# Performance work log

Measured on AMD Instinct MI355X. Metric: run time of the kernel, lower is better.

Reference implementation:

```python
import jax, jax.numpy as jnp
import numpy as np

N_NODES = 100000
N_EDGES = 1600000
IN_DIM = 128
HID = 64
NUM_GRAPHS = 2048
NUM_CLASSES = 1


def setup_inputs() -> dict:
    key = jax.random.key(0)
    ks = jax.random.split(key, 16)
    x = jax.random.normal(ks[0], (N_NODES, IN_DIM), dtype=jnp.float32)
    edge_index = jax.random.randint(ks[1], (2, N_EDGES), 0, N_NODES, dtype=jnp.int64)
    batch_index = jnp.sort(jax.random.randint(ks[2], (N_NODES,), 0, NUM_GRAPHS, dtype=jnp.int64))
    # GCNConv weights (glorot-ish scale)
    def lin(k, fi, fo):
        return jax.random.normal(k, (fi, fo), dtype=jnp.float32) / np.sqrt(fi)
    W1 = lin(ks[3], IN_DIM, HID); b1 = jnp.zeros((HID,), jnp.float32)
    W2 = lin(ks[4], HID, HID);    b2 = jnp.zeros((HID,), jnp.float32)
    W3 = lin(ks[5], HID, HID);    b3 = jnp.zeros((HID,), jnp.float32)
    W4 = lin(ks[6], HID, HID);    b4 = jnp.zeros((HID,), jnp.float32)
    Wout = lin(ks[7], 2 * HID, NUM_CLASSES); bout = jnp.zeros((NUM_CLASSES,), jnp.float32)
    return {"x": x, "edge_index": edge_index, "batch_index": batch_index,
            "W1": W1, "b1": b1, "W2": W2, "b2": b2, "W3": W3, "b3": b3,
            "W4": W4, "b4": b4, "Wout": Wout, "bout": bout}


def _gcn_conv(x, W, b, src, dst, norm, n):
    # PyG GCNConv: linear transform, then D^-1/2 (A+I) D^-1/2 aggregation, then bias
    h = x @ W                                   # [N, F_out]
    msg = h[src] * norm[:, None]                # [E+N, F_out] gather + scale
    agg = jax.ops.segment_sum(msg, dst, num_segments=n)
    return agg + b


def reference(x, edge_index, batch_index, W1, b1, W2, b2, W3, b3, W4, b4, Wout, bout):
    n = x.shape[0]
    loops = jnp.arange(n, dtype=edge_index.dtype)
    src = jnp.concatenate([edge_index[0], loops])  # add self-loops
    dst = jnp.concatenate([edge_index[1], loops])
    deg = jax.ops.segment_sum(jnp.ones_like(dst, dtype=x.dtype), dst, num_segments=n)
    dis = jax.lax.rsqrt(deg)                       # deg >= 1 due to self-loops
    norm = dis[src] * dis[dst]

    h = x
    for (W, b) in ((W1, b1), (W2, b2), (W3, b3), (W4, b4)):
        h = jax.nn.relu(_gcn_conv(h, W, b, src, dst, norm, n))

    # global mean pool + global max pool per graph
    counts = jax.ops.segment_sum(jnp.ones((n,), h.dtype), batch_index, num_segments=NUM_GRAPHS)
    mean = jax.ops.segment_sum(h, batch_index, num_segments=NUM_GRAPHS) / jnp.maximum(counts, 1.0)[:, None]
    mx = jax.ops.segment_max(h, batch_index, num_segments=NUM_GRAPHS)
    mx = jnp.where(counts[:, None] > 0, mx, 0.0)
    pooled = jnp.concatenate([mean, mx], axis=1)   # [G, 2*HID]

    out = pooled @ Wout + bout                     # [G, 1]
    return (out, pooled)
```

## Files before the change

### kernel.cpp

```cpp
#include <hip/hip_runtime.h>
#include <hip/hip_fp16.h>

#define N_NODES 100000
#define IN_DIM 128
#define HID 64
#define NUM_GRAPHS 2048
#define CNE_MAX (1600000 + 7 * N_NODES)
#define BROWS 128
#define NBUCK ((N_NODES + BROWS - 1) / BROWS)
#define NCHUNK 256
#define TOTP (NBUCK * NCHUNK)
#define CAP 4096

typedef _Float16 h8 __attribute__((ext_vector_type(8)));
typedef float f4 __attribute__((ext_vector_type(4)));


__global__ __launch_bounds__(256) void hist_partial(const int* __restrict__ dst,
                                                    int* __restrict__ partial,
                                                    int E, int chunk) {
    __shared__ int lh[NBUCK];
    int t = threadIdx.x, c = blockIdx.x;
    for (int b = t; b < NBUCK; b += 256) lh[b] = 0;
    __syncthreads();
    int lo = c * chunk, hi = min(lo + chunk, E);
    for (int i = lo + t; i < hi; i += 256) atomicAdd(&lh[dst[i] >> 7], 1);
    __syncthreads();
    for (int b = t; b < NBUCK; b += 256) partial[b * NCHUNK + c] = lh[b];
}

__global__ void scan1(const int* __restrict__ counts, int* __restrict__ out1,
                      int* __restrict__ bsum, int n, int pad8) {
    __shared__ int s[256];
    int t = threadIdx.x;
    int base = blockIdx.x * 1024 + t * 4;
    int v[4];
#pragma unroll
    for (int i = 0; i < 4; i++) {
        int c = (base + i < n) ? counts[base + i] : 0;
        v[i] = pad8 ? ((c + 7) & ~7) : c;
    }
    int tsum = v[0] + v[1] + v[2] + v[3];
    s[t] = tsum;
    __syncthreads();
    for (int off = 1; off < 256; off <<= 1) {
        int tv = (t >= off) ? s[t - off] : 0;
        __syncthreads();
        s[t] += tv;
        __syncthreads();
    }
    int excl = s[t] - tsum;
    if (t == 255) bsum[blockIdx.x] = s[255];
    int run = excl;
#pragma unroll
    for (int i = 0; i < 4; i++) {
        run += v[i];
        if (base + i < n) out1[base + i] = run;
    }
}

__global__ void scan2(const int* __restrict__ bsum, int* __restrict__ boff, int nb) {
    __shared__ int s[256];
    int t = threadIdx.x;
    int v = (t < nb) ? bsum[t] : 0;
    s[t] = v;
    __syncthreads();
    for (int off = 1; off < 256; off <<= 1) {
        int tv = (t >= off) ? s[t - off] : 0;
        __syncthreads();
        s[t] += tv;
        __syncthreads();
    }
    if (t < nb) boff[t] = s[t] - v;
}

__global__ void scan3(int* __restrict__ row_ptr, const int* __restrict__ boff, int n) {
    int i = blockIdx.x * blockDim.x + threadIdx.x;
    if (i == 0) row_ptr[0] = 0;
    if (i < n) row_ptr[i + 1] += boff[i >> 10];
}

__global__ void scan3p(const int* __restrict__ partial, const int* __restrict__ pincl,
                       const int* __restrict__ boff, int* __restrict__ base,
                       int* __restrict__ part_off, int E) {
    int i = blockIdx.x * blockDim.x + threadIdx.x;
    if (i < TOTP) {
        int v = pincl[i] + boff[i >> 10] - partial[i];
        base[i] = v;
        if ((i & (NCHUNK - 1)) == 0) part_off[i / NCHUNK] = v;
    }
    if (i == 0) part_off[NBUCK] = E;
}

__global__ __launch_bounds__(256) void partition_edges(const int* __restrict__ src,
                                                       const int* __restrict__ dst,
                                                       const int* __restrict__ base,
                                                       unsigned* __restrict__ part,
                                                       int E, int chunk) {
    __shared__ int cur[NBUCK];
    int t = threadIdx.x, c = blockIdx.x;
    for (int b = t; b < NBUCK; b += 256) cur[b] = base[b * NCHUNK + c];
    __syncthreads();
    int lo = c * chunk, hi = min(lo + chunk, E);
    for (int i = lo + t; i < hi; i += 256) {
        int s = src[i], d = dst[i];
        int pos = atomicAdd(&cur[d >> 7], 1);
        part[pos] = (unsigned)s | ((unsigned)(d & (BROWS - 1)) << 17);
    }
}

__global__ __launch_bounds__(256) void deg_dis(const unsigned* __restrict__ part,
                                               const int* __restrict__ part_off,
                                               int* __restrict__ pdeg,
                                               float* __restrict__ dis, int n) {
    __shared__ int cnt[BROWS];
    int t = threadIdx.x, b = blockIdx.x;
    int r0 = b * BROWS;
    if (t < BROWS) cnt[t] = 0;
    __syncthreads();
    for (int i = part_off[b] + t; i < part_off[b + 1]; i += 256)
        atomicAdd(&cnt[part[i] >> 17], 1);
    __syncthreads();
    int nrows = min(BROWS, n - r0);
    if (t < nrows) {
        int dg = cnt[t];
        pdeg[r0 + t] = dg;
        dis[r0 + t] = rsqrtf((float)(dg + 1));
    }
}

__global__ __launch_bounds__(256) void build_csr(const unsigned* __restrict__ part,
                                                 const int* __restrict__ part_off,
                                                 const int* __restrict__ row_ptr,
                                                 unsigned* __restrict__ cne, int n) {
    __shared__ int fill[BROWS];
    __shared__ unsigned stage[CAP];
    int b = blockIdx.x;
    int r0 = b * BROWS;
    int t = threadIdx.x;
    int nrows = min(BROWS, n - r0);
    int base = row_ptr[r0];
    int region = row_ptr[r0 + nrows] - base;
    for (int r = t; r < nrows; r += 256) fill[r] = row_ptr[r0 + r] - base;
    int i0 = part_off[b], i1 = part_off[b + 1];
    if (region <= CAP) {
        for (int i = t; i < region; i += 256) stage[i] = (unsigned)N_NODES << 7;
        __syncthreads();
        for (int i = i0 + t; i < i1; i += 256) {
            unsigned pe = part[i];
            int pos = atomicAdd(&fill[pe >> 17], 1);
            stage[pos] = (pe & 0x1FFFFu) << 7;
        }
        __syncthreads();
        for (int i = t; i < region; i += 256) cne[base + i] = stage[i];
    } else {
        for (int i = t; i < region; i += 256) cne[base + i] = (unsigned)N_NODES << 7;
        __syncthreads();
        for (int i = i0 + t; i < i1; i += 256) {
            unsigned pe = part[i];
            int pos = atomicAdd(&fill[pe >> 17], 1);
            cne[base + pos] = (pe & 0x1FFFFu) << 7;
        }
    }
}


template <int K, typename XT>
__global__ __launch_bounds__(256) void gemm_mfma(const XT* __restrict__ X,
                                                 const float* __restrict__ W,
                                                 const float* __restrict__ dis,
                                                 __half* __restrict__ out, int n) {
    const int KS = K / 32;
    int wave = threadIdx.x >> 6, lane = threadIdx.x & 63;
    int quad = lane >> 4, l16 = lane & 15;
    h8 b[4][KS];
#pragma unroll
    for (int ct = 0; ct < 4; ct++)
#pragma unroll
        for (int ks = 0; ks < KS; ks++)
#pragma unroll
            for (int j = 0; j < 8; j++)
                b[ct][ks][j] = (_Float16)W[(ks * 32 + quad * 8 + j) * HID + ct * 16 + l16];
    int ntile = n >> 4;
    int wpb = blockDim.x >> 6;
    int stride = gridDim.x * wpb;
    for (int rt = blockIdx.x * wpb + wave; rt < ntile; rt += stride) {
        int row0 = rt << 4;
        const XT* xr = X + (size_t)(row0 + l16) * K + quad * 8;
        f4 acc[4];
#pragma unroll
        for (int ct = 0; ct < 4; ct++) acc[ct] = (f4)(0.f);
#pragma unroll
        for (int ks = 0; ks < KS; ks++) {
            h8 a;
            if constexpr (__is_same(XT, float)) {
                float4 xa = *(const float4*)(xr + ks * 32);
                float4 xb = *(const float4*)(xr + ks * 32 + 4);
                a[0] = (_Float16)xa.x; a[1] = (_Float16)xa.y;
                a[2] = (_Float16)xa.z; a[3] = (_Float16)xa.w;
                a[4] = (_Float16)xb.x; a[5] = (_Float16)xb.y;
                a[6] = (_Float16)xb.z; a[7] = (_Float16)xb.w;
            } else {
                a = *(const h8*)(xr + ks * 32);
            }
#pragma unroll
            for (int ct = 0; ct < 4; ct++)
                acc[ct] = __builtin_amdgcn_mfma_f32_16x16x32_f16(a, b[ct][ks], acc[ct], 0, 0, 0);
        }
        int r0 = row0 + quad * 4;
        float4 dv = *(const float4*)(dis + r0);
        float dd[4] = {dv.x, dv.y, dv.z, dv.w};
#pragma unroll
        for (int reg = 0; reg < 4; reg++) {
            __half* orow = out + (size_t)(r0 + reg) * HID + l16;
            orow[0]  = __float2half(dd[reg] * acc[0][reg]);
            orow[16] = __float2half(dd[reg] * acc[1][reg]);
            orow[32] = __float2half(dd[reg] * acc[2][reg]);
            orow[48] = __float2half(dd[reg] * acc[3][reg]);
        }
    }
}

template <typename OutT>
__global__ __launch_bounds__(256) void aggregate(const __half* __restrict__ tmp,
                                                 const float* __restrict__ dis,
                                                 const int* __restrict__ row_ptr,
                                                 const unsigned* __restrict__ cne,
                                                 const float* __restrict__ bias,
                                                 OutT* __restrict__ out, int n) {
    int wave = threadIdx.x >> 6, lane = threadIdx.x & 63;
    int m = lane & 31, hh = lane >> 5;
    const char* tbase = (const char*)tmp + 4 * m;
    int wpb = blockDim.x >> 6;
    int stride = gridDim.x * wpb;
    float2 blv = *(const float2*)(bias + 2 * m);
    for (int row = blockIdx.x * wpb + wave; row < n; row += stride) {
        float dr = dis[row];
        float ax0 = 0.f, ay0 = 0.f, ax1 = 0.f, ay1 = 0.f;
        float ax2 = 0.f, ay2 = 0.f, ax3 = 0.f, ay3 = 0.f;
        int s = row_ptr[row], e = row_ptr[row + 1];
        int ng = (e - s) >> 3;
        if (ng > 0) {
            const uint4* ip = (const uint4*)(cne + s) + hh;
            uint4 A = ip[0];
            __half2 g0 = *(const __half2*)(tbase + A.x);
            __half2 g1 = *(const __half2*)(tbase + A.y);
            __half2 g2 = *(const __half2*)(tbase + A.z);
            __half2 g3 = *(const __half2*)(tbase + A.w);
            uint4 B;
            if (ng > 1) B = ip[2];
            for (int g = 1; g < ng; g++) {
                __half2 u0 = *(const __half2*)(tbase + B.x);
                __half2 u1 = *(const __half2*)(tbase + B.y);
                __half2 u2 = *(const __half2*)(tbase + B.z);
                __half2 u3 = *(const __half2*)(tbase + B.w);
                if (g + 1 < ng) B = ip[2 * (g + 1)];
                float2 f0 = __half22float2(g0), f1 = __half22float2(g1);
                float2 f2 = __half22float2(g2), f3 = __half22float2(g3);
                ax0 += f0.x; ay0 += f0.y; ax1 += f1.x; ay1 += f1.y;
                ax2 += f2.x; ay2 += f2.y; ax3 += f3.x; ay3 += f3.y;
                g0 = u0; g1 = u1; g2 = u2; g3 = u3;
            }
            float2 f0 = __half22float2(g0), f1 = __half22float2(g1);
            float2 f2 = __half22float2(g2), f3 = __half22float2(g3);
            ax0 += f0.x; ay0 += f0.y; ax1 += f1.x; ay1 += f1.y;
            ax2 += f2.x; ay2 += f2.y; ax3 += f3.x; ay3 += f3.y;
        }
        float sx = (ax0 + ax1) + (ax2 + ax3);
        float sy = (ay0 + ay1) + (ay2 + ay3);
        sx += __shfl_xor(sx, 32);
        sy += __shfl_xor(sy, 32);
        float2 selff = __half22float2(*(const __half2*)(tbase + (size_t)row * 128));
        float rx = fmaxf(dr * (selff.x + sx) + blv.x, 0.f);
        float ry = fmaxf(dr * (selff.y + sy) + blv.y, 0.f);
        if (hh == 0) {
            if constexpr (__is_same(OutT, __half)) {
                *(__half2*)(out + row * HID + 2 * m) = __floats2half2_rn(rx, ry);
            } else {
                *(float2*)(out + row * HID + 2 * m) = make_float2(rx, ry);
            }
        }
    }
}

__global__ __launch_bounds__(256) void pool_kernel(const float* __restrict__ h,
                                                   const int* __restrict__ batch,
                                                   const float* __restrict__ Wout,
                                                   const float* __restrict__ bout,
                                                   float* __restrict__ d_out, int n) {
    __shared__ float ssum[4][64];
    __shared__ float smax[4][64];
    int g = blockIdx.x;
    int wave = threadIdx.x >> 6, j = threadIdx.x & 63;
    int lo = 0, hi = n;
    while (lo < hi) { int mid = (lo + hi) >> 1; if (batch[mid] < g) lo = mid + 1; else hi = mid; }
    int start = lo;
    hi = n;
    while (lo < hi) { int mid = (lo + hi) >> 1; if (batch[mid] < g + 1) lo = mid + 1; else hi = mid; }
    int end = lo;

    float sum = 0.f, mx = 0.f;
    for (int i = start + wave; i < end; i += 4) {
        float v = h[(size_t)i * HID + j];
        sum += v;
        mx = fmaxf(mx, v);
    }
    ssum[wave][j] = sum;
    smax[wave][j] = mx;
    __syncthreads();
    if (wave == 0) {
        sum = (ssum[0][j] + ssum[1][j]) + (ssum[2][j] + ssum[3][j]);
        mx = fmaxf(fmaxf(smax[0][j], smax[1][j]), fmaxf(smax[2][j], smax[3][j]));
        float cnt = (float)(end - start);
        float mean = sum / fmaxf(cnt, 1.f);
        float* pooled = d_out + NUM_GRAPHS;
        pooled[(size_t)g * (2 * HID) + j] = mean;
        pooled[(size_t)g * (2 * HID) + HID + j] = mx;
        float c = mean * Wout[j] + mx * Wout[HID + j];
#pragma unroll
        for (int off = 32; off; off >>= 1) c += __shfl_down(c, off);
        if (j == 0) d_out[g] = c + bout[0];
    }
}


extern "C" void kernel_launch(void* const* d_in, const int* in_sizes, int n_in,
                              void* d_out, int out_size, void* d_ws, size_t ws_size,
                              hipStream_t stream) {
    const float* x    = (const float*)d_in[0];
    const int*   edge = (const int*)d_in[1];
    const int*   batch= (const int*)d_in[2];
    const float* W1 = (const float*)d_in[3];  const float* b1 = (const float*)d_in[4];
    const float* W2 = (const float*)d_in[5];  const float* b2 = (const float*)d_in[6];
    const float* W3 = (const float*)d_in[7];  const float* b3 = (const float*)d_in[8];
    const float* W4 = (const float*)d_in[9];  const float* b4 = (const float*)d_in[10];
    const float* Wout = (const float*)d_in[11]; const float* bout = (const float*)d_in[12];
    float* out = (float*)d_out;

    const int N = N_NODES;
    const int E = in_sizes[1] / 2;
    const int* src = edge;
    const int* dst = edge + E;
    const int chunk = (E + NCHUNK - 1) / NCHUNK;

    char* p = (char*)d_ws;
    auto alloc = [&](size_t bytes) -> char* {
        char* r = p;
        p += (bytes + 255) & ~(size_t)255;
        return r;
    };
    int*      pdeg     = (int*)alloc((size_t)N * 4);
    int*      row_ptr  = (int*)alloc((size_t)(N + 1) * 4);
    int*      partial  = (int*)alloc((size_t)TOTP * 4);
    int*      pincl    = (int*)alloc((size_t)TOTP * 4);
    int*      pbase    = (int*)alloc((size_t)TOTP * 4);
    int*      part_off = (int*)alloc((size_t)(NBUCK + 1) * 4);
    unsigned* part     = (unsigned*)alloc((size_t)1600000 * 4);
    unsigned* cne      = (unsigned*)alloc((size_t)CNE_MAX * 4);
    float*    dis      = (float*)alloc((size_t)N * 4);
    int*      bsum     = (int*)alloc(256 * 4);
    int*      boff     = (int*)alloc(256 * 4);
    __half*   tmp      = (__half*)alloc((size_t)(N + 1) * HID * 2);
    float*    hA       = (float*)alloc((size_t)N * HID * 4);
    __half*   hH       = (__half*)hA;

    hipMemsetAsync(tmp + (size_t)N * HID, 0, HID * 2, stream);

    hist_partial<<<NCHUNK, 256, 0, stream>>>(dst, partial, E, chunk);
    int nbp = (TOTP + 1023) / 1024;
    scan1<<<nbp, 256, 0, stream>>>(partial, pincl, bsum, TOTP, 0);
    scan2<<<1, 256, 0, stream>>>(bsum, boff, nbp);
    scan3p<<<(TOTP + 255) / 256, 256, 0, stream>>>(partial, pincl, boff, pbase, part_off, E);
    partition_edges<<<NCHUNK, 256, 0, stream>>>(src, dst, pbase, part, E, chunk);
    deg_dis<<<NBUCK, 256, 0, stream>>>(part, part_off, pdeg, dis, N);

    int nb = (N + 1023) / 1024;
    scan1<<<nb, 256, 0, stream>>>(pdeg, row_ptr + 1, bsum, N, 1);
    scan2<<<1, 256, 0, stream>>>(bsum, boff, nb);
    scan3<<<(N + 255) / 256, 256, 0, stream>>>(row_ptr, boff, N);
    build_csr<<<NBUCK, 256, 0, stream>>>(part, part_off, row_ptr, cne, N);

    const int AGG_BLOCKS = 2048;
    const int GEMM_BLOCKS = 1024;

    gemm_mfma<IN_DIM, float><<<GEMM_BLOCKS, 256, 0, stream>>>(x, W1, dis, tmp, N);
    aggregate<__half><<<AGG_BLOCKS, 256, 0, stream>>>(tmp, dis, row_ptr, cne, b1, hH, N);
    gemm_mfma<HID, _Float16><<<GEMM_BLOCKS, 256, 0, stream>>>((_Float16*)hH, W2, dis, tmp, N);
    aggregate<__half><<<AGG_BLOCKS, 256, 0, stream>>>(tmp, dis, row_ptr, cne, b2, hH, N);
    gemm_mfma<HID, _Float16><<<GEMM_BLOCKS, 256, 0, stream>>>((_Float16*)hH, W3, dis, tmp, N);
    aggregate<__half><<<AGG_BLOCKS, 256, 0, stream>>>(tmp, dis, row_ptr, cne, b3, hH, N);
    gemm_mfma<HID, _Float16><<<GEMM_BLOCKS, 256, 0, stream>>>((_Float16*)hH, W4, dis, tmp, N);
    aggregate<float><<<AGG_BLOCKS, 256, 0, stream>>>(tmp, dis, row_ptr, cne, b4, hA, N);

    pool_kernel<<<NUM_GRAPHS, 256, 0, stream>>>(hA, batch, Wout, bout, out, N);
}
```

Baseline: 358.4 us.

## Fuse aggregation with next-layer MFMA GEMM and fold scan2 into consumers

Each middle GCN layer's neighbor aggregation now writes its ReLU output tile of 16 rows into shared memory, then multiplies it by the next layer's weight with MFMA in the same kernel. This drops the round trip of the intermediate hidden activations through global memory and removes three launches. The single-block scan2 kernel is folded into scan3 and scan3p, and the pad-row memset is moved into hist_partial, which cuts more launches. In exchange, every block redundantly rescans the block sums, the fused kernel adds two __syncthreads per tile, it assumes N is a multiple of 16, and it does less aggregation work per block than the previous separate kernels.

```diff
diff --git a/kernel.cpp b/kernel.cpp
--- a/kernel.cpp
+++ b/kernel.cpp
@@ -18,9 +18,15 @@
 
 __global__ __launch_bounds__(256) void hist_partial(const int* __restrict__ dst,
                                                     int* __restrict__ partial,
-                                                    int E, int chunk) {
+                                                    int E, int chunk,
+                                                    unsigned* __restrict__ padA,
+                                                    unsigned* __restrict__ padB) {
     __shared__ int lh[NBUCK];
     int t = threadIdx.x, c = blockIdx.x;
+    if (c == 0) {
+        if (t < 32) padA[t] = 0;
+        else if (t < 64) padB[t - 32] = 0;
+    }
     for (int b = t; b < NBUCK; b += 256) lh[b] = 0;
     __syncthreads();
     int lo = c * chunk, hi = min(lo + chunk, E);
@@ -59,8 +65,7 @@
     }
 }
 
-__global__ void scan2(const int* __restrict__ bsum, int* __restrict__ boff, int nb) {
-    __shared__ int s[256];
+__device__ __forceinline__ int inline_bscan(const int* __restrict__ bsum, int nb, int* s) {
     int t = threadIdx.x;
     int v = (t < nb) ? bsum[t] : 0;
     s[t] = v;
@@ -71,21 +76,32 @@
         s[t] += tv;
         __syncthreads();
     }
-    if (t < nb) boff[t] = s[t] - v;
-}
-
-__global__ void scan3(int* __restrict__ row_ptr, const int* __restrict__ boff, int n) {
+    int excl = s[t] - v;
+    __syncthreads();
+    s[t] = excl;
+    __syncthreads();
+    return excl;
+}
+
+__global__ __launch_bounds__(256) void scan3(int* __restrict__ row_ptr,
+                                             const int* __restrict__ bsum, int nb, int n) {
+    __shared__ int s[256];
+    inline_bscan(bsum, nb, s);
     int i = blockIdx.x * blockDim.x + threadIdx.x;
     if (i == 0) row_ptr[0] = 0;
-    if (i < n) row_ptr[i + 1] += boff[i >> 10];
-}
-
-__global__ void scan3p(const int* __restrict__ partial, const int* __restrict__ pincl,
-                       const int* __restrict__ boff, int* __restrict__ base,
-                       int* __restrict__ part_off, int E) {
+    if (i < n) row_ptr[i + 1] += s[i >> 10];
+}
+
+__global__ __launch_bounds__(256) void scan3p(const int* __restrict__ partial,
+                                              const int* __restrict__ pincl,
+                                              const int* __restrict__ bsum, int nb,
+                                              int* __restrict__ base,
+                                              int* __restrict__ part_off, int E) {
+    __shared__ int s[256];
+    inline_bscan(bsum, nb, s);
     int i = blockIdx.x * blockDim.x + threadIdx.x;
     if (i < TOTP) {
-        int v = pincl[i] + boff[i >> 10] - partial[i];
+        int v = pincl[i] + s[i >> 10] - partial[i];
         base[i] = v;
         if ((i & (NCHUNK - 1)) == 0) part_off[i / NCHUNK] = v;
     }
@@ -283,6 +299,86 @@
     }
 }
 
+__global__ __launch_bounds__(256) void fused_agg_gemm(const __half* __restrict__ tmp,
+                                                      const float* __restrict__ dis,
+                                                      const int* __restrict__ row_ptr,
+                                                      const unsigned* __restrict__ cne,
+                                                      const float* __restrict__ bias,
+                                                      const float* __restrict__ W,
+                                                      __half* __restrict__ out, int n) {
+    __shared__ __half hs[16][72];
+    int wave = threadIdx.x >> 6, lane = threadIdx.x & 63;
+    int m = lane & 31, hh = lane >> 5;
+    int quad = lane >> 4, l16 = lane & 15;
+    const char* tbase = (const char*)tmp + 4 * m;
+    float2 blv = *(const float2*)(bias + 2 * m);
+    h8 b0, b1;
+#pragma unroll
+    for (int j = 0; j < 8; j++) {
+        b0[j] = (_Float16)W[(quad * 8 + j) * HID + wave * 16 + l16];
+        b1[j] = (_Float16)W[(32 + quad * 8 + j) * HID + wave * 16 + l16];
+    }
+    int ntile = n >> 4;
+    for (int rt = blockIdx.x; rt < ntile; rt += gridDim.x) {
+        int r0 = rt << 4;
+        for (int i = 0; i < 4; i++) {
+            int row = r0 + (wave << 2) + i;
+            float dr = dis[row];
+            float ax0 = 0.f, ay0 = 0.f, ax1 = 0.f, ay1 = 0.f;
+            float ax2 = 0.f, ay2 = 0.f, ax3 = 0.f, ay3 = 0.f;
+            int s_ = row_ptr[row], e_ = row_ptr[row + 1];
+            int ng = (e_ - s_) >> 3;
+            if (ng > 0) {
+                const uint4* ip = (const uint4*)(cne + s_) + hh;
+                uint4 A = ip[0];
+                __half2 g0 = *(const __half2*)(tbase + A.x);
+                __half2 g1 = *(const __half2*)(tbase + A.y);
+                __half2 g2 = *(const __half2*)(tbase + A.z);
+                __half2 g3 = *(const __half2*)(tbase + A.w);
+                uint4 B;
+                if (ng > 1) B = ip[2];
+                for (int g = 1; g < ng; g++) {
+                    __half2 u0 = *(const __half2*)(tbase + B.x);
+                    __half2 u1 = *(const __half2*)(tbase + B.y);
+                    __half2 u2 = *(const __half2*)(tbase + B.z);
+                    __half2 u3 = *(const __half2*)(tbase + B.w);
+                    if (g + 1 < ng) B = ip[2 * (g + 1)];
+                    float2 f0 = __half22float2(g0), f1 = __half22float2(g1);
+                    float2 f2 = __half22float2(g2), f3 = __half22float2(g3);
+                    ax0 += f0.x; ay0 += f0.y; ax1 += f1.x; ay1 += f1.y;
+                    ax2 += f2.x; ay2 += f2.y; ax3 += f3.x; ay3 += f3.y;
+                    g0 = u0; g1 = u1; g2 = u2; g3 = u3;
+                }
+                float2 f0 = __half22float2(g0), f1 = __half22float2(g1);
+                float2 f2 = __half22float2(g2), f3 = __half22float2(g3);
+                ax0 += f0.x; ay0 += f0.y; ax1 += f1.x; ay1 += f1.y;
+                ax2 += f2.x; ay2 += f2.y; ax3 += f3.x; ay3 += f3.y;
+            }
+            float sx = (ax0 + ax1) + (ax2 + ax3);
+            float sy = (ay0 + ay1) + (ay2 + ay3);
+            sx += __shfl_xor(sx, 32);
+            sy += __shfl_xor(sy, 32);
+            float2 selff = __half22float2(*(const __half2*)(tbase + (size_t)row * 128));
+            float rx = fmaxf(dr * (selff.x + sx) + blv.x, 0.f);
+            float ry = fmaxf(dr * (selff.y + sy) + blv.y, 0.f);
+            if (hh == 0) *(__half2*)&hs[(wave << 2) + i][2 * m] = __floats2half2_rn(rx, ry);
+        }
+        __syncthreads();
+        f4 acc = (f4)(0.f);
+        h8 a0 = *(const h8*)&hs[l16][quad * 8];
+        h8 a1 = *(const h8*)&hs[l16][32 + quad * 8];
+        acc = __builtin_amdgcn_mfma_f32_16x16x32_f16(a0, b0, acc, 0, 0, 0);
+        acc = __builtin_amdgcn_mfma_f32_16x16x32_f16(a1, b1, acc, 0, 0, 0);
+        int rr = r0 + quad * 4;
+        float4 dv = *(const float4*)(dis + rr);
+        float dd[4] = {dv.x, dv.y, dv.z, dv.w};
+#pragma unroll
+        for (int reg = 0; reg < 4; reg++)
+            out[(size_t)(rr + reg) * HID + wave * 16 + l16] = __float2half(dd[reg] * acc[reg]);
+        __syncthreads();
+    }
+}
+
 __global__ __launch_bounds__(256) void pool_kernel(const float* __restrict__ h,
                                                    const int* __restrict__ batch,
                                                    const float* __restrict__ Wout,
@@ -359,38 +455,32 @@
     unsigned* cne      = (unsigned*)alloc((size_t)CNE_MAX * 4);
     float*    dis      = (float*)alloc((size_t)N * 4);
     int*      bsum     = (int*)alloc(256 * 4);
-    int*      boff     = (int*)alloc(256 * 4);
-    __half*   tmp      = (__half*)alloc((size_t)(N + 1) * HID * 2);
+    __half*   tmpA     = (__half*)alloc((size_t)(N + 1) * HID * 2);
+    __half*   tmpB     = (__half*)alloc((size_t)(N + 1) * HID * 2);
     float*    hA       = (float*)alloc((size_t)N * HID * 4);
-    __half*   hH       = (__half*)hA;
-
-    hipMemsetAsync(tmp + (size_t)N * HID, 0, HID * 2, stream);
-
-    hist_partial<<<NCHUNK, 256, 0, stream>>>(dst, partial, E, chunk);
+
+    hist_partial<<<NCHUNK, 256, 0, stream>>>(dst, partial, E, chunk,
+                                             (unsigned*)(tmpA + (size_t)N * HID),
+                                             (unsigned*)(tmpB + (size_t)N * HID));
     int nbp = (TOTP + 1023) / 1024;
     scan1<<<nbp, 256, 0, stream>>>(partial, pincl, bsum, TOTP, 0);
-    scan2<<<1, 256, 0, stream>>>(bsum, boff, nbp);
-    scan3p<<<(TOTP + 255) / 256, 256, 0, stream>>>(partial, pincl, boff, pbase, part_off, E);
+    scan3p<<<(TOTP + 255) / 256, 256, 0, stream>>>(partial, pincl, bsum, nbp, pbase, part_off, E);
     partition_edges<<<NCHUNK, 256, 0, stream>>>(src, dst, pbase, part, E, chunk);
     deg_dis<<<NBUCK, 256, 0, stream>>>(part, part_off, pdeg, dis, N);
 
     int nb = (N + 1023) / 1024;
     scan1<<<nb, 256, 0, stream>>>(pdeg, row_ptr + 1, bsum, N, 1);
-    scan2<<<1, 256, 0, stream>>>(bsum, boff, nb);
-    scan3<<<(N + 255) / 256, 256, 0, stream>>>(row_ptr, boff, N);
+    scan3<<<(N + 255) / 256, 256, 0, stream>>>(row_ptr, bsum, nb, N);
     build_csr<<<NBUCK, 256, 0, stream>>>(part, part_off, row_ptr, cne, N);
 
     const int AGG_BLOCKS = 2048;
     const int GEMM_BLOCKS = 1024;
 
-    gemm_mfma<IN_DIM, float><<<GEMM_BLOCKS, 256, 0, stream>>>(x, W1, dis, tmp, N);
-    aggregate<__half><<<AGG_BLOCKS, 256, 0, stream>>>(tmp, dis, row_ptr, cne, b1, hH, N);
-    gemm_mfma<HID, _Float16><<<GEMM_BLOCKS, 256, 0, stream>>>((_Float16*)hH, W2, dis, tmp, N);
-    aggregate<__half><<<AGG_BLOCKS, 256, 0, stream>>>(tmp, dis, row_ptr, cne, b2, hH, N);
-    gemm_mfma<HID, _Float16><<<GEMM_BLOCKS, 256, 0, stream>>>((_Float16*)hH, W3, dis, tmp, N);
-    aggregate<__half><<<AGG_BLOCKS, 256, 0, stream>>>(tmp, dis, row_ptr, cne, b3, hH, N);
-    gemm_mfma<HID, _Float16><<<GEMM_BLOCKS, 256, 0, stream>>>((_Float16*)hH, W4, dis, tmp, N);
-    aggregate<float><<<AGG_BLOCKS, 256, 0, stream>>>(tmp, dis, row_ptr, cne, b4, hA, N);
+    gemm_mfma<IN_DIM, float><<<GEMM_BLOCKS, 256, 0, stream>>>(x, W1, dis, tmpA, N);
+    fused_agg_gemm<<<AGG_BLOCKS, 256, 0, stream>>>(tmpA, dis, row_ptr, cne, b1, W2, tmpB, N);
+    fused_agg_gemm<<<AGG_BLOCKS, 256, 0, stream>>>(tmpB, dis, row_ptr, cne, b2, W3, tmpA, N);
+    fused_agg_gemm<<<AGG_BLOCKS, 256, 0, stream>>>(tmpA, dis, row_ptr, cne, b3, W4, tmpB, N);
+    aggregate<float><<<AGG_BLOCKS, 256, 0, stream>>>(tmpB, dis, row_ptr, cne, b4, hA, N);
 
     pool_kernel<<<NUM_GRAPHS, 256, 0, stream>>>(hA, batch, Wout, bout, out, N);
 }
```

Measured after the change: 380.7 us. 6.2% more time.

## Process two rows per wave in aggregation and fold scan2 into consumers

Applied to the files above, without the earlier changes.

The aggregate kernel now gives each half-wave its own destination row, so one wave handles two rows and each half-wave walks all eight neighbor indices of a group instead of splitting them and merging with a cross-half shuffle. The separate single-block scan2 launches are removed; each scan3/scan3p block recomputes the block-offset scan in shared memory. The pad-row memset is folded into the hist_partial kernel. This cuts launch count and the per-row shuffle, at the cost of unequal row lengths within a wave causing divergence, and redundant small scans in every block. The pair loop uses n>>1, so an odd final row would be skipped; this is harmless only because N is even.

```diff
diff --git a/kernel.cpp b/kernel.cpp
--- a/kernel.cpp
+++ b/kernel.cpp
@@ -18,9 +18,15 @@
 
 __global__ __launch_bounds__(256) void hist_partial(const int* __restrict__ dst,
                                                     int* __restrict__ partial,
-                                                    int E, int chunk) {
+                                                    int E, int chunk,
+                                                    unsigned* __restrict__ padA,
+                                                    unsigned* __restrict__ padB) {
     __shared__ int lh[NBUCK];
     int t = threadIdx.x, c = blockIdx.x;
+    if (c == 0) {
+        if (t < 32) padA[t] = 0;
+        else if (t < 64) padB[t - 32] = 0;
+    }
     for (int b = t; b < NBUCK; b += 256) lh[b] = 0;
     __syncthreads();
     int lo = c * chunk, hi = min(lo + chunk, E);
@@ -59,8 +65,7 @@
     }
 }
 
-__global__ void scan2(const int* __restrict__ bsum, int* __restrict__ boff, int nb) {
-    __shared__ int s[256];
+__device__ __forceinline__ int inline_bscan(const int* __restrict__ bsum, int nb, int* s) {
     int t = threadIdx.x;
     int v = (t < nb) ? bsum[t] : 0;
     s[t] = v;
@@ -71,21 +76,32 @@
         s[t] += tv;
         __syncthreads();
     }
-    if (t < nb) boff[t] = s[t] - v;
-}
-
-__global__ void scan3(int* __restrict__ row_ptr, const int* __restrict__ boff, int n) {
+    int excl = s[t] - v;
+    __syncthreads();
+    s[t] = excl;
+    __syncthreads();
+    return excl;
+}
+
+__global__ __launch_bounds__(256) void scan3(int* __restrict__ row_ptr,
+                                             const int* __restrict__ bsum, int nb, int n) {
+    __shared__ int s[256];
+    inline_bscan(bsum, nb, s);
     int i = blockIdx.x * blockDim.x + threadIdx.x;
     if (i == 0) row_ptr[0] = 0;
-    if (i < n) row_ptr[i + 1] += boff[i >> 10];
-}
-
-__global__ void scan3p(const int* __restrict__ partial, const int* __restrict__ pincl,
-                       const int* __restrict__ boff, int* __restrict__ base,
-                       int* __restrict__ part_off, int E) {
+    if (i < n) row_ptr[i + 1] += s[i >> 10];
+}
+
+__global__ __launch_bounds__(256) void scan3p(const int* __restrict__ partial,
+                                              const int* __restrict__ pincl,
+                                              const int* __restrict__ bsum, int nb,
+                                              int* __restrict__ base,
+                                              int* __restrict__ part_off, int E) {
+    __shared__ int s[256];
+    inline_bscan(bsum, nb, s);
     int i = blockIdx.x * blockDim.x + threadIdx.x;
     if (i < TOTP) {
-        int v = pincl[i] + boff[i >> 10] - partial[i];
+        int v = pincl[i] + s[i >> 10] - partial[i];
         base[i] = v;
         if ((i & (NCHUNK - 1)) == 0) part_off[i / NCHUNK] = v;
     }
@@ -222,63 +238,78 @@
 }
 
 template <typename OutT>
-__global__ __launch_bounds__(256) void aggregate(const __half* __restrict__ tmp,
-                                                 const float* __restrict__ dis,
-                                                 const int* __restrict__ row_ptr,
-                                                 const unsigned* __restrict__ cne,
-                                                 const float* __restrict__ bias,
-                                                 OutT* __restrict__ out, int n) {
+__global__ __launch_bounds__(256) void aggregate2(const __half* __restrict__ tmp,
+                                                  const float* __restrict__ dis,
+                                                  const int* __restrict__ row_ptr,
+                                                  const unsigned* __restrict__ cne,
+                                                  const float* __restrict__ bias,
+                                                  OutT* __restrict__ out, int n) {
     int wave = threadIdx.x >> 6, lane = threadIdx.x & 63;
     int m = lane & 31, hh = lane >> 5;
     const char* tbase = (const char*)tmp + 4 * m;
     int wpb = blockDim.x >> 6;
     int stride = gridDim.x * wpb;
     float2 blv = *(const float2*)(bias + 2 * m);
-    for (int row = blockIdx.x * wpb + wave; row < n; row += stride) {
+    int npairs = n >> 1;
+    for (int p = blockIdx.x * wpb + wave; p < npairs; p += stride) {
+        int row = 2 * p + hh;
         float dr = dis[row];
+        int s = row_ptr[row], e = row_ptr[row + 1];
+        int ng = (e - s) >> 3;
         float ax0 = 0.f, ay0 = 0.f, ax1 = 0.f, ay1 = 0.f;
         float ax2 = 0.f, ay2 = 0.f, ax3 = 0.f, ay3 = 0.f;
-        int s = row_ptr[row], e = row_ptr[row + 1];
-        int ng = (e - s) >> 3;
         if (ng > 0) {
-            const uint4* ip = (const uint4*)(cne + s) + hh;
-            uint4 A = ip[0];
-            __half2 g0 = *(const __half2*)(tbase + A.x);
-            __half2 g1 = *(const __half2*)(tbase + A.y);
-            __half2 g2 = *(const __half2*)(tbase + A.z);
-            __half2 g3 = *(const __half2*)(tbase + A.w);
-            uint4 B;
-            if (ng > 1) B = ip[2];
+            const uint4* ip = (const uint4*)(cne + s);
+            uint4 A0 = ip[0], A1 = ip[1];
+            __half2 g0 = *(const __half2*)(tbase + A0.x);
+            __half2 g1 = *(const __half2*)(tbase + A0.y);
+            __half2 g2 = *(const __half2*)(tbase + A0.z);
+            __half2 g3 = *(const __half2*)(tbase + A0.w);
+            __half2 g4 = *(const __half2*)(tbase + A1.x);
+            __half2 g5 = *(const __half2*)(tbase + A1.y);
+            __half2 g6 = *(const __half2*)(tbase + A1.z);
+            __half2 g7 = *(const __half2*)(tbase + A1.w);
+            uint4 B0, B1;
+            if (ng > 1) { B0 = ip[2]; B1 = ip[3]; }
             for (int g = 1; g < ng; g++) {
-                __half2 u0 = *(const __half2*)(tbase + B.x);
-                __half2 u1 = *(const __half2*)(tbase + B.y);
-                __half2 u2 = *(const __half2*)(tbase + B.z);
-                __half2 u3 = *(const __half2*)(tbase + B.w);
-                if (g + 1 < ng) B = ip[2 * (g + 1)];
+                __half2 u0 = *(const __half2*)(tbase + B0.x);
+                __half2 u1 = *(const __half2*)(tbase + B0.y);
+                __half2 u2 = *(const __half2*)(tbase + B0.z);
+                __half2 u3 = *(const __half2*)(tbase + B0.w);
+                __half2 u4 = *(const __half2*)(tbase + B1.x);
+                __half2 u5 = *(const __half2*)(tbase + B1.y);
+                __half2 u6 = *(const __half2*)(tbase + B1.z);
+                __half2 u7 = *(const __half2*)(tbase + B1.w);
+                if (g + 1 < ng) { B0 = ip[2 * (g + 1)]; B1 = ip[2 * (g + 1) + 1]; }
                 float2 f0 = __half22float2(g0), f1 = __half22float2(g1);
                 float2 f2 = __half22float2(g2), f3 = __half22float2(g3);
+                float2 f4 = __half22float2(g4), f5 = __half22float2(g5);
+                float2 f6 = __half22float2(g6), f7 = __half22float2(g7);
                 ax0 += f0.x; ay0 += f0.y; ax1 += f1.x; ay1 += f1.y;
                 ax2 += f2.x; ay2 += f2.y; ax3 += f3.x; ay3 += f3.y;
+                ax0 += f4.x; ay0 += f4.y; ax1 += f5.x; ay1 += f5.y;
+                ax2 += f6.x; ay2 += f6.y; ax3 += f7.x; ay3 += f7.y;
                 g0 = u0; g1 = u1; g2 = u2; g3 = u3;
+                g4 = u4; g5 = u5; g6 = u6; g7 = u7;
             }
             float2 f0 = __half22float2(g0), f1 = __half22float2(g1);
             float2 f2 = __half22float2(g2), f3 = __half22float2(g3);
+            float2 f4 = __half22float2(g4), f5 = __half22float2(g5);
+            float2 f6 = __half22float2(g6), f7 = __half22float2(g7);
             ax0 += f0.x; ay0 += f0.y; ax1 += f1.x; ay1 += f1.y;
             ax2 += f2.x; ay2 += f2.y; ax3 += f3.x; ay3 += f3.y;
+            ax0 += f4.x; ay0 += f4.y; ax1 += f5.x; ay1 += f5.y;
+            ax2 += f6.x; ay2 += f6.y; ax3 += f7.x; ay3 += f7.y;
         }
         float sx = (ax0 + ax1) + (ax2 + ax3);
         float sy = (ay0 + ay1) + (ay2 + ay3);
-        sx += __shfl_xor(sx, 32);
-        sy += __shfl_xor(sy, 32);
         float2 selff = __half22float2(*(const __half2*)(tbase + (size_t)row * 128));
         float rx = fmaxf(dr * (selff.x + sx) + blv.x, 0.f);
         float ry = fmaxf(dr * (selff.y + sy) + blv.y, 0.f);
-        if (hh == 0) {
-            if constexpr (__is_same(OutT, __half)) {
-                *(__half2*)(out + row * HID + 2 * m) = __floats2half2_rn(rx, ry);
-            } else {
-                *(float2*)(out + row * HID + 2 * m) = make_float2(rx, ry);
-            }
+        if constexpr (__is_same(OutT, __half)) {
+            *(__half2*)(out + (size_t)row * HID + 2 * m) = __floats2half2_rn(rx, ry);
+        } else {
+            *(float2*)(out + (size_t)row * HID + 2 * m) = make_float2(rx, ry);
         }
     }
 }
@@ -359,38 +390,34 @@
     unsigned* cne      = (unsigned*)alloc((size_t)CNE_MAX * 4);
     float*    dis      = (float*)alloc((size_t)N * 4);
     int*      bsum     = (int*)alloc(256 * 4);
-    int*      boff     = (int*)alloc(256 * 4);
     __half*   tmp      = (__half*)alloc((size_t)(N + 1) * HID * 2);
     float*    hA       = (float*)alloc((size_t)N * HID * 4);
     __half*   hH       = (__half*)hA;
 
-    hipMemsetAsync(tmp + (size_t)N * HID, 0, HID * 2, stream);
-
-    hist_partial<<<NCHUNK, 256, 0, stream>>>(dst, partial, E, chunk);
+    unsigned* padrow = (unsigned*)(tmp + (size_t)N * HID);
+    hist_partial<<<NCHUNK, 256, 0, stream>>>(dst, partial, E, chunk, padrow, padrow);
     int nbp = (TOTP + 1023) / 1024;
     scan1<<<nbp, 256, 0, stream>>>(partial, pincl, bsum, TOTP, 0);
-    scan2<<<1, 256, 0, stream>>>(bsum, boff, nbp);
-    scan3p<<<(TOTP + 255) / 256, 256, 0, stream>>>(partial, pincl, boff, pbase, part_off, E);
+    scan3p<<<(TOTP + 255) / 256, 256, 0, stream>>>(partial, pincl, bsum, nbp, pbase, part_off, E);
     partition_edges<<<NCHUNK, 256, 0, stream>>>(src, dst, pbase, part, E, chunk);
     deg_dis<<<NBUCK, 256, 0, stream>>>(part, part_off, pdeg, dis, N);
 
     int nb = (N + 1023) / 1024;
     scan1<<<nb, 256, 0, stream>>>(pdeg, row_ptr + 1, bsum, N, 1);
-    scan2<<<1, 256, 0, stream>>>(bsum, boff, nb);
-    scan3<<<(N + 255) / 256, 256, 0, stream>>>(row_ptr, boff, N);
+    scan3<<<(N + 255) / 256, 256, 0, stream>>>(row_ptr, bsum, nb, N);
     build_csr<<<NBUCK, 256, 0, stream>>>(part, part_off, row_ptr, cne, N);
 
     const int AGG_BLOCKS = 2048;
     const int GEMM_BLOCKS = 1024;
 
     gemm_mfma<IN_DIM, float><<<GEMM_BLOCKS, 256, 0, stream>>>(x, W1, dis, tmp, N);
-    aggregate<__half><<<AGG_BLOCKS, 256, 0, stream>>>(tmp, dis, row_ptr, cne, b1, hH, N);
+    aggregate2<__half><<<AGG_BLOCKS, 256, 0, stream>>>(tmp, dis, row_ptr, cne, b1, hH, N);
     gemm_mfma<HID, _Float16><<<GEMM_BLOCKS, 256, 0, stream>>>((_Float16*)hH, W2, dis, tmp, N);
-    aggregate<__half><<<AGG_BLOCKS, 256, 0, stream>>>(tmp, dis, row_ptr, cne, b2, hH, N);
+    aggregate2<__half><<<AGG_BLOCKS, 256, 0, stream>>>(tmp, dis, row_ptr, cne, b2, hH, N);
     gemm_mfma<HID, _Float16><<<GEMM_BLOCKS, 256, 0, stream>>>((_Float16*)hH, W3, dis, tmp, N);
-    aggregate<__half><<<AGG_BLOCKS, 256, 0, stream>>>(tmp, dis, row_ptr, cne, b3, hH, N);
+    aggregate2<__half><<<AGG_BLOCKS, 256, 0, stream>>>(tmp, dis, row_ptr, cne, b3, hH, N);
     gemm_mfma<HID, _Float16><<<GEMM_BLOCKS, 256, 0, stream>>>((_Float16*)hH, W4, dis, tmp, N);
-    aggregate<float><<<AGG_BLOCKS, 256, 0, stream>>>(tmp, dis, row_ptr, cne, b4, hA, N);
+    aggregate2<float><<<AGG_BLOCKS, 256, 0, stream>>>(tmp, dis, row_ptr, cne, b4, hA, N);
 
     pool_kernel<<<NUM_GRAPHS, 256, 0, stream>>>(hA, batch, Wout, bout, out, N);
 }
```

Result: faster. 343.2 us (-4.2%).
